# Kernel tuning notes

Measured on AMD Instinct MI355X. Metric: run time of the kernel, lower is better.

The kernel has to match this reference:

```python
import jax, jax.numpy as jnp
import numpy as np
from jax import lax

DIM = 128
HEADS = 8
B, H, W = 8, 128, 128


def conv1x1(w, x):
    # w: [out_c, in_c], x: [b, in_c, h, w]
    return jnp.einsum('oc,bchw->bohw', w, x)


def setup_inputs() -> dict:
    key = jax.random.key(0)
    ks = jax.random.split(key, 12)
    s = 0.02
    return {
        'x': jax.random.normal(ks[0], (B, DIM, H, W), dtype=jnp.float32),
        'W_qkv': jax.random.normal(ks[1], (3 * DIM, DIM), dtype=jnp.float32) * s,
        'W_dw': jax.random.normal(ks[2], (DIM, 1, 3, 3), dtype=jnp.float32) * s,
        'W_proj_s': jax.random.normal(ks[3], (DIM, DIM), dtype=jnp.float32) * s,
        'scale_s': jnp.ones((HEADS, 1, 1), dtype=jnp.float32),
        'W_ff1': jax.random.normal(ks[4], (DIM, DIM), dtype=jnp.float32) * s,
        'W_ff2': jax.random.normal(ks[5], (DIM, DIM), dtype=jnp.float32) * s,
        'W_proj_f': jax.random.normal(ks[6], (DIM, DIM), dtype=jnp.float32) * s,
        'W_gsf': jax.random.normal(ks[7], (DIM, DIM), dtype=jnp.float32) * s,
        'b_gsf': jnp.zeros((DIM,), dtype=jnp.float32),
        'W_gfs': jax.random.normal(ks[8], (DIM, DIM), dtype=jnp.float32) * s,
        'b_gfs': jnp.zeros((DIM,), dtype=jnp.float32),
    }


def reference(x, W_qkv, W_dw, W_proj_s, scale_s, W_ff1, W_ff2, W_proj_f,
              W_gsf, b_gsf, W_gfs, b_gfs):
    b, c, h, w = x.shape
    head = HEADS
    ch = c // head

    # --- channel self-attention branch ---
    qkv = conv1x1(W_qkv, x)                      # [b, 3c, h, w]
    q_s, k_s, v_s = jnp.split(qkv, 3, axis=1)
    v_s_conv = lax.conv_general_dilated(
        v_s, W_dw, window_strides=(1, 1), padding='SAME',
        feature_group_count=c,
        dimension_numbers=('NCHW', 'OIHW', 'NCHW'))  # depthwise 3x3

    q = q_s.reshape(b, head, ch, h * w)
    k = k_s.reshape(b, head, ch, h * w)
    v = v_s.reshape(b, head, ch, h * w)
    attn = jax.nn.softmax(jnp.einsum('bhcn,bhdn->bhcd', q, k) * scale_s, axis=-1)
    out_s = jnp.einsum('bhcd,bhdn->bhcn', attn, v).reshape(b, c, h, w)
    out_s = conv1x1(W_proj_s, out_s + v_s_conv)

    # --- frequency filter branch ---
    xf = jnp.fft.rfft2(x, norm='ortho')          # complex [b,c,h,w//2+1]
    spatial_weights = conv1x1(W_ff2, jax.nn.gelu(conv1x1(W_ff1, x), approximate=False))
    freq_weights = jnp.fft.rfft2(spatial_weights, norm='ortho')
    out_f = jnp.fft.irfft2(xf * freq_weights, s=(h, w), norm='ortho')
    out_f = conv1x1(W_proj_f, out_f)

    # --- sigmoid-gated fusion ---
    gate_f = jax.nn.sigmoid(conv1x1(W_gsf, out_s) + b_gsf[:, None, None])
    gate_s = jax.nn.sigmoid(conv1x1(W_gfs, out_f) + b_gfs[:, None, None])
    return x + out_s * gate_s + out_f * gate_f
```

## Files before the change

kernel.cpp:

```cpp
#include <hip/hip_runtime.h>
#include <hip/hip_bf16.h>
#include <math.h>

#define HW 16384

typedef __attribute__((ext_vector_type(8))) short bf16x8;
typedef __attribute__((ext_vector_type(4))) float f32x4;

__device__ __forceinline__ unsigned short f2bf(float a)
{
    __hip_bfloat16 h = __float2bfloat16(a);
    return __builtin_bit_cast(unsigned short, h);
}
__device__ __forceinline__ unsigned f2bf_pk(float a, float b)
{
    return (unsigned)f2bf(a) | ((unsigned)f2bf(b) << 16);
}
__device__ __forceinline__ float bf2f(unsigned short u)
{
    return __uint_as_float(((unsigned)u) << 16);
}
__device__ __forceinline__ float sigmoidf_(float v) { return 1.f / (1.f + expf(-v)); }

__device__ __forceinline__ float2 cmul(float2 a, float2 b)
{
    return make_float2(a.x * b.x - a.y * b.y, a.x * b.y + a.y * b.x);
}

__global__ __launch_bounds__(256)
void wprep_k(const float* __restrict__ w0, const float* __restrict__ w1,
             const float* __restrict__ w2, const float* __restrict__ w3,
             const float* __restrict__ w4, const float* __restrict__ w5,
             const float* __restrict__ w6, int4* __restrict__ Wbf4)
{
    int m = blockIdx.x >> 3;
    int slot = (blockIdx.x & 7) * 256 + threadIdx.x;
    const float* src;
    switch (m) {
        case 0: src = w0; break;
        case 1: src = w1; break;
        case 2: src = w2; break;
        case 3: src = w3; break;
        case 4: src = w4; break;
        case 5: src = w5; break;
        default: src = w6; break;
    }
    int o = slot >> 4;
    int c16 = (slot & 15) ^ (o & 7);
    const float* p = src + o * 128 + c16 * 8;
    int4 pk;
    pk.x = f2bf_pk(p[0], p[1]); pk.y = f2bf_pk(p[2], p[3]);
    pk.z = f2bf_pk(p[4], p[5]); pk.w = f2bf_pk(p[6], p[7]);
    Wbf4[m * 2048 + slot] = pk;
}

__global__ __launch_bounds__(256)
void conv_mfma_k(const float* __restrict__ in, const int4* __restrict__ wbf,
                 unsigned short* __restrict__ out)
{
    __shared__ short WL[128 * 128];
    __shared__ short XL[64 * 128];
    int t = threadIdx.x;
    int gb = blockIdx.x;
    int b = gb >> 8;
    int n0 = (gb & 255) << 6;

    #pragma unroll
    for (int it = 0; it < 8; ++it)
        ((int4*)WL)[it * 256 + t] = wbf[it * 256 + t];

    const float* inb = in + (size_t)b * 128 * HW + n0;
    int nl = t & 63;
    #pragma unroll
    for (int it = 0; it < 4; ++it) {
        int c8 = (t >> 6) + it * 4;
        float v[8];
        #pragma unroll
        for (int j = 0; j < 8; ++j) v[j] = inb[(size_t)(c8 * 8 + j) * HW + nl];
        int4 p;
        p.x = f2bf_pk(v[0], v[1]); p.y = f2bf_pk(v[2], v[3]);
        p.z = f2bf_pk(v[4], v[5]); p.w = f2bf_pk(v[6], v[7]);
        ((int4*)XL)[nl * 16 + (c8 ^ (nl & 7))] = p;
    }
    __syncthreads();

    int l = t & 63, w = t >> 6, kg = l >> 4, l15 = l & 15, l7 = l15 & 7;
    f32x4 acc[2][4];
    #pragma unroll
    for (int mf = 0; mf < 2; ++mf)
        #pragma unroll
        for (int nf = 0; nf < 4; ++nf) acc[mf][nf] = (f32x4){0.f, 0.f, 0.f, 0.f};
    #pragma unroll
    for (int ks = 0; ks < 4; ++ks) {
        int ch = ks * 4 + kg;
        bf16x8 A0 = ((const bf16x8*)WL)[(w * 32 + l15) * 16 + (ch ^ l7)];
        bf16x8 A1 = ((const bf16x8*)WL)[(w * 32 + 16 + l15) * 16 + (ch ^ l7)];
        #pragma unroll
        for (int nf = 0; nf < 4; ++nf) {
            bf16x8 Bf = ((const bf16x8*)XL)[(nf * 16 + l15) * 16 + (ch ^ l7)];
            acc[0][nf] = __builtin_amdgcn_mfma_f32_16x16x32_bf16(A0, Bf, acc[0][nf], 0, 0, 0);
            acc[1][nf] = __builtin_amdgcn_mfma_f32_16x16x32_bf16(A1, Bf, acc[1][nf], 0, 0, 0);
        }
    }
    #pragma unroll
    for (int mf = 0; mf < 2; ++mf)
        #pragma unroll
        for (int nf = 0; nf < 4; ++nf)
            #pragma unroll
            for (int i = 0; i < 4; ++i) {
                int row = w * 32 + mf * 16 + kg * 4 + i;
                int col = n0 + nf * 16 + l15;
                out[((size_t)b * 128 + row) * HW + col] = f2bf(acc[mf][nf][i]);
            }
}

__global__ __launch_bounds__(256)
void conv_mfma_bf_k(const unsigned short* __restrict__ in,
                    const int4* __restrict__ wbf,
                    unsigned short* __restrict__ out)
{
    __shared__ short WL[128 * 128];
    __shared__ short XL[64 * 128];
    int t = threadIdx.x;
    int gb = blockIdx.x;
    int b = gb >> 8;
    int n0 = (gb & 255) << 6;

    #pragma unroll
    for (int it = 0; it < 8; ++it)
        ((int4*)WL)[it * 256 + t] = wbf[it * 256 + t];

    const unsigned short* inb = in + (size_t)b * 128 * HW + n0;
    int nl = t & 63;
    #pragma unroll
    for (int it = 0; it < 4; ++it) {
        int c8 = (t >> 6) + it * 4;
        unsigned u[8];
        #pragma unroll
        for (int j = 0; j < 8; ++j) u[j] = inb[(size_t)(c8 * 8 + j) * HW + nl];
        int4 p;
        p.x = (int)(u[0] | (u[1] << 16)); p.y = (int)(u[2] | (u[3] << 16));
        p.z = (int)(u[4] | (u[5] << 16)); p.w = (int)(u[6] | (u[7] << 16));
        ((int4*)XL)[nl * 16 + (c8 ^ (nl & 7))] = p;
    }
    __syncthreads();

    int l = t & 63, w = t >> 6, kg = l >> 4, l15 = l & 15, l7 = l15 & 7;
    f32x4 acc[2][4];
    #pragma unroll
    for (int mf = 0; mf < 2; ++mf)
        #pragma unroll
        for (int nf = 0; nf < 4; ++nf) acc[mf][nf] = (f32x4){0.f, 0.f, 0.f, 0.f};
    #pragma unroll
    for (int ks = 0; ks < 4; ++ks) {
        int ch = ks * 4 + kg;
        bf16x8 A0 = ((const bf16x8*)WL)[(w * 32 + l15) * 16 + (ch ^ l7)];
        bf16x8 A1 = ((const bf16x8*)WL)[(w * 32 + 16 + l15) * 16 + (ch ^ l7)];
        #pragma unroll
        for (int nf = 0; nf < 4; ++nf) {
            bf16x8 Bf = ((const bf16x8*)XL)[(nf * 16 + l15) * 16 + (ch ^ l7)];
            acc[0][nf] = __builtin_amdgcn_mfma_f32_16x16x32_bf16(A0, Bf, acc[0][nf], 0, 0, 0);
            acc[1][nf] = __builtin_amdgcn_mfma_f32_16x16x32_bf16(A1, Bf, acc[1][nf], 0, 0, 0);
        }
    }
    #pragma unroll
    for (int mf = 0; mf < 2; ++mf)
        #pragma unroll
        for (int nf = 0; nf < 4; ++nf)
            #pragma unroll
            for (int i = 0; i < 4; ++i) {
                int row = w * 32 + mf * 16 + kg * 4 + i;
                int col = n0 + nf * 16 + l15;
                out[((size_t)b * 128 + row) * HW + col] = f2bf(acc[mf][nf][i]);
            }
}

__global__ __launch_bounds__(256)
void dwconv_k(const unsigned short* __restrict__ V, const float* __restrict__ Wdw,
              unsigned short* __restrict__ vcb)
{
    int tid = blockIdx.x * 256 + threadIdx.x;
    int e4 = tid & 4095;
    int bc = tid >> 12;
    int c = bc & 127;
    int y = e4 >> 5;
    int x0 = (e4 & 31) << 2;
    const unsigned short* vin = V + (size_t)bc * HW;
    float wf[9];
    #pragma unroll
    for (int i = 0; i < 9; ++i) wf[i] = Wdw[c * 9 + i];
    float a0 = 0.f, a1 = 0.f, a2 = 0.f, a3 = 0.f;
    #pragma unroll
    for (int dy = 0; dy < 3; ++dy) {
        int yy = y + dy - 1;
        if (yy < 0 || yy > 127) continue;
        const unsigned short* r = vin + yy * 128;
        uint2 mu = *(const uint2*)(r + x0);
        float m0 = bf2f((unsigned short)(mu.x & 0xFFFF));
        float m1 = bf2f((unsigned short)(mu.x >> 16));
        float m2 = bf2f((unsigned short)(mu.y & 0xFFFF));
        float m3 = bf2f((unsigned short)(mu.y >> 16));
        float left  = (x0 > 0)   ? bf2f(r[x0 - 1]) : 0.f;
        float right = (x0 < 124) ? bf2f(r[x0 + 4]) : 0.f;
        float w0 = wf[dy * 3], w1 = wf[dy * 3 + 1], w2 = wf[dy * 3 + 2];
        a0 += w0 * left + w1 * m0 + w2 * m1;
        a1 += w0 * m0   + w1 * m1 + w2 * m2;
        a2 += w0 * m1   + w1 * m2 + w2 * m3;
        a3 += w0 * m2   + w1 * m3 + w2 * right;
    }
    uint2 r2;
    r2.x = f2bf_pk(a0, a1);
    r2.y = f2bf_pk(a2, a3);
    *(uint2*)(vcb + (size_t)bc * HW + y * 128 + x0) = r2;
}

__global__ __launch_bounds__(256)
void gram_mfma_k(const float* __restrict__ x, float* __restrict__ Gp)
{
    __shared__ short XL[128 * 128];
    int t = threadIdx.x;
    int blk = blockIdx.x;
    int b = blk >> 5, ks = blk & 31;
    const float* xb = x + (size_t)b * 128 * HW + ks * 512;
    int l = t & 63, w = t >> 6, kg = l >> 4, l15 = l & 15, l7 = l15 & 7;

    f32x4 acc[2][8];
    #pragma unroll
    for (int mf = 0; mf < 2; ++mf)
        #pragma unroll
        for (int nf = 0; nf < 8; ++nf) acc[mf][nf] = (f32x4){0.f, 0.f, 0.f, 0.f};

    for (int kc = 0; kc < 4; ++kc) {
        __syncthreads();
        #pragma unroll
        for (int it = 0; it < 8; ++it) {
            int g = it * 256 + t;
            int row = g >> 4, oct = g & 15;
            const float* p = xb + (size_t)row * HW + kc * 128 + oct * 8;
            int4 pk;
            pk.x = f2bf_pk(p[0], p[1]); pk.y = f2bf_pk(p[2], p[3]);
            pk.z = f2bf_pk(p[4], p[5]); pk.w = f2bf_pk(p[6], p[7]);
            ((int4*)XL)[row * 16 + (oct ^ (row & 7))] = pk;
        }
        __syncthreads();
        #pragma unroll
        for (int s = 0; s < 4; ++s) {
            int oct = s * 4 + kg;
            bf16x8 A0 = ((const bf16x8*)XL)[(w * 32 + l15) * 16 + (oct ^ l7)];
            bf16x8 A1 = ((const bf16x8*)XL)[(w * 32 + 16 + l15) * 16 + (oct ^ l7)];
            #pragma unroll
            for (int nf = 0; nf < 8; ++nf) {
                bf16x8 Bf = ((const bf16x8*)XL)[(nf * 16 + l15) * 16 + (oct ^ l7)];
                acc[0][nf] = __builtin_amdgcn_mfma_f32_16x16x32_bf16(A0, Bf, acc[0][nf], 0, 0, 0);
                acc[1][nf] = __builtin_amdgcn_mfma_f32_16x16x32_bf16(A1, Bf, acc[1][nf], 0, 0, 0);
            }
        }
    }
    float* gp = Gp + (size_t)blk * 16384;
    #pragma unroll
    for (int mf = 0; mf < 2; ++mf)
        #pragma unroll
        for (int nf = 0; nf < 8; ++nf)
            #pragma unroll
            for (int i = 0; i < 4; ++i) {
                int row = w * 32 + mf * 16 + kg * 4 + i;
                int col = nf * 16 + l15;
                gp[row * 128 + col] = acc[mf][nf][i];
            }
}

__global__ void gram_reduce_k(const float* __restrict__ Gp, float* __restrict__ G)
{
    int idx = blockIdx.x * 256 + threadIdx.x;
    int b = idx >> 14;
    int ij = idx & 16383;
    const float* gp = Gp + (size_t)(b * 32) * 16384 + ij;
    float s = 0.f;
    #pragma unroll
    for (int ks = 0; ks < 32; ++ks) s += gp[(size_t)ks * 16384];
    G[idx] = s;
}

__global__ __launch_bounds__(256)
void attn_s2_k(const float* __restrict__ G, const float* __restrict__ Wqkv,
               const float* __restrict__ scale, float* __restrict__ S)
{
    __shared__ float Wq[16][129];
    __shared__ float Wk[16][129];
    __shared__ float Ts[16][129];
    int bh = blockIdx.x;
    int b = bh >> 3, h = bh & 7;
    int t = threadIdx.x;
    #pragma unroll
    for (int i = 0; i < 8; ++i) {
        int idx = t + i * 256;
        int r = idx >> 7, ci = idx & 127;
        Wq[r][ci] = Wqkv[(size_t)(h * 16 + r) * 128 + ci];
        Wk[r][ci] = Wqkv[(size_t)(128 + h * 16 + r) * 128 + ci];
    }
    __syncthreads();
    const float* Gb = G + (size_t)b * 16384;
    #pragma unroll
    for (int i = 0; i < 8; ++i) {
        int idx = t + i * 256;
        int c = idx >> 7, col = idx & 127;
        float s = 0.f;
        #pragma unroll 8
        for (int ci = 0; ci < 128; ++ci)
            s += Wq[c][ci] * Gb[ci * 128 + col];
        Ts[c][col] = s;
    }
    __syncthreads();
    int c = t >> 4, d = t & 15;
    float s = 0.f;
    #pragma unroll 8
    for (int col = 0; col < 128; ++col)
        s += Ts[c][col] * Wk[d][col];
    s *= scale[h];
    float m = s;
    #pragma unroll
    for (int w = 1; w < 16; w <<= 1)
        m = fmaxf(m, __shfl_xor(m, w, 64));
    float e = expf(s - m);
    float sum = e;
    #pragma unroll
    for (int w = 1; w < 16; w <<= 1)
        sum += __shfl_xor(sum, w, 64);
    S[(size_t)bh * 256 + t] = e / sum;
}

__global__ __launch_bounds__(256)
void proj_s_pv_k(const unsigned short* __restrict__ V,
                 const unsigned short* __restrict__ vcb,
                 const float* __restrict__ S, const int4* __restrict__ wbf,
                 unsigned short* __restrict__ out_s)
{
    __shared__ short WL[128 * 128];
    __shared__ short XL[64 * 128];
    __shared__ float SL[2048];
    int t = threadIdx.x;
    int gb = blockIdx.x;
    int b = gb >> 8;
    int n0 = (gb & 255) << 6;

    #pragma unroll
    for (int it = 0; it < 8; ++it)
        ((int4*)WL)[it * 256 + t] = wbf[it * 256 + t];
    #pragma unroll
    for (int i = 0; i < 8; ++i)
        SL[i * 256 + t] = S[(size_t)b * 2048 + i * 256 + t];
    __syncthreads();

    int col = t & 63, w = t >> 6;
    #pragma unroll
    for (int hh = 0; hh < 2; ++hh) {
        int h = w * 2 + hh;
        float v[16];
        #pragma unroll
        for (int d = 0; d < 16; ++d)
            v[d] = bf2f(V[((size_t)(b * 128 + h * 16 + d)) * HW + n0 + col]);
        float o[16];
        #pragma unroll
        for (int c = 0; c < 16; ++c) {
            const float* sl = SL + h * 256 + c * 16;
            float s = 0.f;
            #pragma unroll
            for (int d = 0; d < 16; ++d) s += sl[d] * v[d];
            o[c] = s + bf2f(vcb[((size_t)(b * 128 + h * 16 + c)) * HW + n0 + col]);
        }
        #pragma unroll
        for (int oc = 0; oc < 2; ++oc) {
            int octet = h * 2 + oc;
            int4 p;
            p.x = f2bf_pk(o[oc * 8 + 0], o[oc * 8 + 1]);
            p.y = f2bf_pk(o[oc * 8 + 2], o[oc * 8 + 3]);
            p.z = f2bf_pk(o[oc * 8 + 4], o[oc * 8 + 5]);
            p.w = f2bf_pk(o[oc * 8 + 6], o[oc * 8 + 7]);
            ((int4*)XL)[col * 16 + (octet ^ (col & 7))] = p;
        }
    }
    __syncthreads();

    int l = t & 63, kg = l >> 4, l15 = l & 15, l7 = l15 & 7;
    f32x4 acc[2][4];
    #pragma unroll
    for (int mf = 0; mf < 2; ++mf)
        #pragma unroll
        for (int nf = 0; nf < 4; ++nf) acc[mf][nf] = (f32x4){0.f, 0.f, 0.f, 0.f};
    #pragma unroll
    for (int ks = 0; ks < 4; ++ks) {
        int ch = ks * 4 + kg;
        bf16x8 A0 = ((const bf16x8*)WL)[(w * 32 + l15) * 16 + (ch ^ l7)];
        bf16x8 A1 = ((const bf16x8*)WL)[(w * 32 + 16 + l15) * 16 + (ch ^ l7)];
        #pragma unroll
        for (int nf = 0; nf < 4; ++nf) {
            bf16x8 Bf = ((const bf16x8*)XL)[(nf * 16 + l15) * 16 + (ch ^ l7)];
            acc[0][nf] = __builtin_amdgcn_mfma_f32_16x16x32_bf16(A0, Bf, acc[0][nf], 0, 0, 0);
            acc[1][nf] = __builtin_amdgcn_mfma_f32_16x16x32_bf16(A1, Bf, acc[1][nf], 0, 0, 0);
        }
    }
    #pragma unroll
    for (int mf = 0; mf < 2; ++mf)
        #pragma unroll
        for (int nf = 0; nf < 4; ++nf)
            #pragma unroll
            for (int i = 0; i < 4; ++i) {
                int row = w * 32 + mf * 16 + kg * 4 + i;
                int colg = n0 + nf * 16 + l15;
                out_s[((size_t)b * 128 + row) * HW + colg] = f2bf(acc[mf][nf][i]);
            }
}

__global__ __launch_bounds__(256)
void ff_fused_k(const float* __restrict__ x, const int4* __restrict__ w1bf,
                const int4* __restrict__ w2bf, unsigned short* __restrict__ outp)
{
    __shared__ short WL[128 * 128];
    __shared__ short XL[64 * 128];
    int t = threadIdx.x;
    int gb = blockIdx.x;
    int b = gb >> 8;
    int n0 = (gb & 255) << 6;

    #pragma unroll
    for (int it = 0; it < 8; ++it)
        ((int4*)WL)[it * 256 + t] = w1bf[it * 256 + t];

    const float* inb = x + (size_t)b * 128 * HW + n0;
    int nl = t & 63;
    #pragma unroll
    for (int it = 0; it < 4; ++it) {
        int c8 = (t >> 6) + it * 4;
        float v[8];
        #pragma unroll
        for (int j = 0; j < 8; ++j) v[j] = inb[(size_t)(c8 * 8 + j) * HW + nl];
        int4 p;
        p.x = f2bf_pk(v[0], v[1]); p.y = f2bf_pk(v[2], v[3]);
        p.z = f2bf_pk(v[4], v[5]); p.w = f2bf_pk(v[6], v[7]);
        ((int4*)XL)[nl * 16 + (c8 ^ (nl & 7))] = p;
    }
    __syncthreads();

    int l = t & 63, w = t >> 6, kg = l >> 4, l15 = l & 15, l7 = l15 & 7;
    f32x4 acc[2][4];
    #pragma unroll
    for (int mf = 0; mf < 2; ++mf)
        #pragma unroll
        for (int nf = 0; nf < 4; ++nf) acc[mf][nf] = (f32x4){0.f, 0.f, 0.f, 0.f};
    #pragma unroll
    for (int ks = 0; ks < 4; ++ks) {
        int ch = ks * 4 + kg;
        bf16x8 A0 = ((const bf16x8*)WL)[(w * 32 + l15) * 16 + (ch ^ l7)];
        bf16x8 A1 = ((const bf16x8*)WL)[(w * 32 + 16 + l15) * 16 + (ch ^ l7)];
        #pragma unroll
        for (int nf = 0; nf < 4; ++nf) {
            bf16x8 Bf = ((const bf16x8*)XL)[(nf * 16 + l15) * 16 + (ch ^ l7)];
            acc[0][nf] = __builtin_amdgcn_mfma_f32_16x16x32_bf16(A0, Bf, acc[0][nf], 0, 0, 0);
            acc[1][nf] = __builtin_amdgcn_mfma_f32_16x16x32_bf16(A1, Bf, acc[1][nf], 0, 0, 0);
        }
    }
    __syncthreads();

    #pragma unroll
    for (int it = 0; it < 8; ++it)
        ((int4*)WL)[it * 256 + t] = w2bf[it * 256 + t];
    #pragma unroll
    for (int mf = 0; mf < 2; ++mf)
        #pragma unroll
        for (int nf = 0; nf < 4; ++nf) {
            float g4[4];
            #pragma unroll
            for (int i = 0; i < 4; ++i) {
                float v = acc[mf][nf][i];
                g4[i] = 0.5f * v * (1.0f + erff(v * 0.70710678118654752f));
            }
            int col = nf * 16 + l15;
            int r0 = w * 32 + mf * 16 + kg * 4;
            int octet = r0 >> 3;
            uint2 pk2;
            pk2.x = f2bf_pk(g4[0], g4[1]);
            pk2.y = f2bf_pk(g4[2], g4[3]);
            ((uint2*)XL)[(col * 16 + (octet ^ (col & 7))) * 2 + (kg & 1)] = pk2;
        }
    __syncthreads();

    f32x4 acc2[2][4];
    #pragma unroll
    for (int mf = 0; mf < 2; ++mf)
        #pragma unroll
        for (int nf = 0; nf < 4; ++nf) acc2[mf][nf] = (f32x4){0.f, 0.f, 0.f, 0.f};
    #pragma unroll
    for (int ks = 0; ks < 4; ++ks) {
        int ch = ks * 4 + kg;
        bf16x8 A0 = ((const bf16x8*)WL)[(w * 32 + l15) * 16 + (ch ^ l7)];
        bf16x8 A1 = ((const bf16x8*)WL)[(w * 32 + 16 + l15) * 16 + (ch ^ l7)];
        #pragma unroll
        for (int nf = 0; nf < 4; ++nf) {
            bf16x8 Bf = ((const bf16x8*)XL)[(nf * 16 + l15) * 16 + (ch ^ l7)];
            acc2[0][nf] = __builtin_amdgcn_mfma_f32_16x16x32_bf16(A0, Bf, acc2[0][nf], 0, 0, 0);
            acc2[1][nf] = __builtin_amdgcn_mfma_f32_16x16x32_bf16(A1, Bf, acc2[1][nf], 0, 0, 0);
        }
    }
    #pragma unroll
    for (int mf = 0; mf < 2; ++mf)
        #pragma unroll
        for (int nf = 0; nf < 4; ++nf)
            #pragma unroll
            for (int i = 0; i < 4; ++i) {
                int row = w * 32 + mf * 16 + kg * 4 + i;
                int col = n0 + nf * 16 + l15;
                outp[((size_t)b * 128 + row) * HW + col] = f2bf(acc2[mf][nf][i]);
            }
}

__global__ __launch_bounds__(256)
void fuse2_k(const float* __restrict__ x, const unsigned short* __restrict__ outs,
             const unsigned short* __restrict__ outf,
             const int4* __restrict__ wgsf_bf, const float* __restrict__ bgsf,
             const int4* __restrict__ wgfs_bf, const float* __restrict__ bgfs,
             float* __restrict__ out)
{
    __shared__ short WS[64 * 128];
    __shared__ short WF[64 * 128];
    __shared__ short XS[64 * 128];
    __shared__ short XF[64 * 128];
    int t = threadIdx.x;
    int gb = blockIdx.x;
    int half = gb & 1;
    int nt = (gb >> 1) & 255;
    int b = gb >> 9;
    int n0 = nt << 6;

    #pragma unroll
    for (int it = 0; it < 4; ++it) {
        ((int4*)WS)[it * 256 + t] = wgsf_bf[half * 1024 + it * 256 + t];
        ((int4*)WF)[it * 256 + t] = wgfs_bf[half * 1024 + it * 256 + t];
    }
    const unsigned short* sb = outs + (size_t)b * 128 * HW + n0;
    const unsigned short* fb = outf + (size_t)b * 128 * HW + n0;
    int nl = t & 63;
    #pragma unroll
    for (int it = 0; it < 4; ++it) {
        int c8 = (t >> 6) + it * 4;
        unsigned us[8], uf[8];
        #pragma unroll
        for (int j = 0; j < 8; ++j) {
            size_t a = (size_t)(c8 * 8 + j) * HW + nl;
            us[j] = sb[a];
            uf[j] = fb[a];
        }
        int4 ps, pf;
        ps.x = (int)(us[0] | (us[1] << 16)); ps.y = (int)(us[2] | (us[3] << 16));
        ps.z = (int)(us[4] | (us[5] << 16)); ps.w = (int)(us[6] | (us[7] << 16));
        pf.x = (int)(uf[0] | (uf[1] << 16)); pf.y = (int)(uf[2] | (uf[3] << 16));
        pf.z = (int)(uf[4] | (uf[5] << 16)); pf.w = (int)(uf[6] | (uf[7] << 16));
        ((int4*)XS)[nl * 16 + (c8 ^ (nl & 7))] = ps;
        ((int4*)XF)[nl * 16 + (c8 ^ (nl & 7))] = pf;
    }
    __syncthreads();

    int l = t & 63, w = t >> 6, kg = l >> 4, l15 = l & 15, l7 = l15 & 7;
    f32x4 aS[4], aF[4];
    #pragma unroll
    for (int nf = 0; nf < 4; ++nf) {
        aS[nf] = (f32x4){0.f, 0.f, 0.f, 0.f};
        aF[nf] = (f32x4){0.f, 0.f, 0.f, 0.f};
    }
    #pragma unroll
    for (int ks = 0; ks < 4; ++ks) {
        int ch = ks * 4 + kg;
        bf16x8 As = ((const bf16x8*)WS)[(w * 16 + l15) * 16 + (ch ^ l7)];
        bf16x8 Af = ((const bf16x8*)WF)[(w * 16 + l15) * 16 + (ch ^ l7)];
        #pragma unroll
        for (int nf = 0; nf < 4; ++nf) {
            bf16x8 Bs = ((const bf16x8*)XS)[(nf * 16 + l15) * 16 + (ch ^ l7)];
            bf16x8 Bf = ((const bf16x8*)XF)[(nf * 16 + l15) * 16 + (ch ^ l7)];
            aS[nf] = __builtin_amdgcn_mfma_f32_16x16x32_bf16(As, Bs, aS[nf], 0, 0, 0);
            aF[nf] = __builtin_amdgcn_mfma_f32_16x16x32_bf16(Af, Bf, aF[nf], 0, 0, 0);
        }
    }
    #pragma unroll
    for (int nf = 0; nf < 4; ++nf)
        #pragma unroll
        for (int i = 0; i < 4; ++i) {
            int row = half * 64 + w * 16 + kg * 4 + i;
            int cc = nf * 16 + l15;
            float gf = sigmoidf_(aS[nf][i] + bgsf[row]);
            float gs = sigmoidf_(aF[nf][i] + bgfs[row]);
            size_t gi = ((size_t)(b * 128) + row) * HW + n0 + cc;
            float os = bf2f(outs[gi]);
            float of = bf2f(outf[gi]);
            out[gi] = x[gi] + os * gs + of * gf;
        }
}

__device__ __forceinline__ int ZIX(int r, int j)
{
    return r * 128 + (j ^ ((r & 3) << 3) ^ (((j >> 4) & 3) << 1));
}
__device__ __forceinline__ float2 zld(const unsigned* Z, int r, int j)
{
    unsigned z = Z[ZIX(r, j)];
    return make_float2(bf2f((unsigned short)(z & 0xFFFF)),
                       bf2f((unsigned short)(z >> 16)));
}
__device__ __forceinline__ void zst(unsigned* Z, int r, int j, float2 v)
{
    Z[ZIX(r, j)] = f2bf_pk(v.x, v.y);
}

__device__ __forceinline__ void dft16(float2* v)
{
    const float C1 = 0.92387953251f, S1 = 0.38268343236f, R2 = 0.70710678119f;
    const float2 W16[8] = {
        {1.f, 0.f}, {C1, -S1}, {R2, -R2}, {S1, -C1},
        {0.f, -1.f}, {-S1, -C1}, {-R2, -R2}, {-C1, -S1}};
    #pragma unroll
    for (int i = 0; i < 8; ++i) {
        float2 a = v[i], b = v[i + 8];
        v[i] = make_float2(a.x + b.x, a.y + b.y);
        float2 d = make_float2(a.x - b.x, a.y - b.y);
        v[i + 8] = cmul(d, W16[i]);
    }
    #pragma unroll
    for (int blk = 0; blk < 16; blk += 8)
        #pragma unroll
        for (int i = 0; i < 4; ++i) {
            float2 a = v[blk + i], b = v[blk + i + 4];
            v[blk + i] = make_float2(a.x + b.x, a.y + b.y);
            float2 d = make_float2(a.x - b.x, a.y - b.y);
            v[blk + i + 4] = cmul(d, W16[2 * i]);
        }
    #pragma unroll
    for (int blk = 0; blk < 16; blk += 4) {
        float2 a0 = v[blk], b0 = v[blk + 2];
        v[blk] = make_float2(a0.x + b0.x, a0.y + b0.y);
        v[blk + 2] = make_float2(a0.x - b0.x, a0.y - b0.y);
        float2 a1 = v[blk + 1], b1 = v[blk + 3];
        v[blk + 1] = make_float2(a1.x + b1.x, a1.y + b1.y);
        float2 d = make_float2(a1.x - b1.x, a1.y - b1.y);
        v[blk + 3] = make_float2(d.y, -d.x);
    }
    #pragma unroll
    for (int blk = 0; blk < 16; blk += 2) {
        float2 a = v[blk], b = v[blk + 1];
        v[blk] = make_float2(a.x + b.x, a.y + b.y);
        v[blk + 1] = make_float2(a.x - b.x, a.y - b.y);
    }
}

__device__ __forceinline__ void dft8(float2* v)
{
    const float R2 = 0.70710678119f;
    const float2 W8[4] = {{1.f, 0.f}, {R2, -R2}, {0.f, -1.f}, {-R2, -R2}};
    #pragma unroll
    for (int i = 0; i < 4; ++i) {
        float2 a = v[i], b = v[i + 4];
        v[i] = make_float2(a.x + b.x, a.y + b.y);
        float2 d = make_float2(a.x - b.x, a.y - b.y);
        v[i + 4] = cmul(d, W8[i]);
    }
    #pragma unroll
    for (int blk = 0; blk < 8; blk += 4) {
        float2 a0 = v[blk], b0 = v[blk + 2];
        v[blk] = make_float2(a0.x + b0.x, a0.y + b0.y);
        v[blk + 2] = make_float2(a0.x - b0.x, a0.y - b0.y);
        float2 a1 = v[blk + 1], b1 = v[blk + 3];
        v[blk + 1] = make_float2(a1.x + b1.x, a1.y + b1.y);
        float2 d = make_float2(a1.x - b1.x, a1.y - b1.y);
        v[blk + 3] = make_float2(d.y, -d.x);
    }
    #pragma unroll
    for (int blk = 0; blk < 8; blk += 2) {
        float2 a = v[blk], b = v[blk + 1];
        v[blk] = make_float2(a.x + b.x, a.y + b.y);
        v[blk + 1] = make_float2(a.x - b.x, a.y - b.y);
    }
}

__device__ __forceinline__ void fft_line_row(unsigned* Z, const float2* tw,
                                             int row, int n2)
{
    const int BREV4[16] = {0,8,4,12,2,10,6,14,1,9,5,13,3,11,7,15};
    const int BREV3[8] = {0,4,2,6,1,5,3,7};
    float2 v[16];
    #pragma unroll
    for (int n1 = 0; n1 < 16; ++n1) v[n1] = zld(Z, row, 8 * n1 + n2);
    dft16(v);
    #pragma unroll
    for (int p = 0; p < 16; ++p) {
        int k1 = BREV4[p];
        zst(Z, row, 16 * n2 + k1, cmul(v[p], tw[n2 * k1]));
    }
    float2 wa[8], wb[8];
    #pragma unroll
    for (int m = 0; m < 8; ++m) {
        wa[m] = zld(Z, row, 16 * m + n2);
        wb[m] = zld(Z, row, 16 * m + n2 + 8);
    }
    dft8(wa);
    dft8(wb);
    #pragma unroll
    for (int p = 0; p < 8; ++p) {
        zst(Z, row, n2 + 16 * BREV3[p], wa[p]);
        zst(Z, row, n2 + 8 + 16 * BREV3[p], wb[p]);
    }
}

__device__ __forceinline__ void fft_line_col(unsigned* Z, const float2* tw,
                                             int col, int n2)
{
    const int BREV4[16] = {0,8,4,12,2,10,6,14,1,9,5,13,3,11,7,15};
    const int BREV3[8] = {0,4,2,6,1,5,3,7};
    float2 v[16];
    #pragma unroll
    for (int n1 = 0; n1 < 16; ++n1) v[n1] = zld(Z, 8 * n1 + n2, col);
    dft16(v);
    #pragma unroll
    for (int p = 0; p < 16; ++p) {
        int k1 = BREV4[p];
        zst(Z, 16 * n2 + k1, col, cmul(v[p], tw[n2 * k1]));
    }
    float2 wa[8], wb[8];
    #pragma unroll
    for (int m = 0; m < 8; ++m) {
        wa[m] = zld(Z, 16 * m + n2, col);
        wb[m] = zld(Z, 16 * m + n2 + 8, col);
    }
    dft8(wa);
    dft8(wb);
    #pragma unroll
    for (int p = 0; p < 8; ++p) {
        zst(Z, n2 + 16 * BREV3[p], col, wa[p]);
        zst(Z, n2 + 8 + 16 * BREV3[p], col, wb[p]);
    }
}

__global__ __launch_bounds__(256)
void fft_all_k(const float* __restrict__ x, const unsigned short* __restrict__ sw,
               unsigned short* __restrict__ outp)
{
    __shared__ unsigned Z[128 * 128];
    __shared__ float2 tw[128];
    const int BREV3[8] = {0,4,2,6,1,5,3,7};
    int t = threadIdx.x;
    if (t < 128) {
        float sn, cs;
        sincosf(0.049087385212340519f * (float)t, &sn, &cs);
        tw[t] = make_float2(cs, -sn);
    }
    size_t base = (size_t)blockIdx.x * HW;

    for (int i = 0; i < 64; ++i) {
        int idx = t + i * 256;
        int r = idx >> 7, j = idx & 127;
        Z[ZIX(r, j)] = (unsigned)f2bf(x[base + idx]) |
                       ((unsigned)sw[base + idx] << 16);
    }
    __syncthreads();

    int ln = t >> 3, n2 = t & 7;
    #pragma unroll
    for (int it = 0; it < 4; ++it) fft_line_row(Z, tw, it * 32 + ln, n2);
    __syncthreads();
    #pragma unroll
    for (int it = 0; it < 4; ++it) fft_line_col(Z, tw, it * 32 + ln, n2);
    __syncthreads();

    for (int item = t; item < 8194; item += 256) {
        int rA, kA, rB, kB;
        if (item < 8064) {
            rA = 1 + (item >> 7); kA = item & 127;
            rB = 128 - rA; kB = (128 - kA) & 127;
        } else {
            int it2 = item - 8064;
            rA = rB = (it2 < 65) ? 0 : 64;
            kA = (it2 < 65) ? it2 : (it2 - 65);
            kB = (128 - kA) & 127;
        }
        float2 z1 = zld(Z, rA, kA);
        float2 z2 = zld(Z, rB, kB);
        float2 X = make_float2(0.5f * (z1.x + z2.x), 0.5f * (z1.y - z2.y));
        float Dx = z1.x - z2.x, Dy = z1.y + z2.y;
        float2 Wf = make_float2(0.5f * Dy, -0.5f * Dx);
        float2 Y = cmul(X, Wf);
        zst(Z, rA, kA, make_float2(Y.x, -Y.y));
        zst(Z, rB, kB, Y);
    }
    __syncthreads();

    #pragma unroll
    for (int it = 0; it < 4; ++it) fft_line_col(Z, tw, it * 32 + ln, n2);
    __syncthreads();

    const float scale = 1.f / 2097152.f;
    const int BREV4[16] = {0,8,4,12,2,10,6,14,1,9,5,13,3,11,7,15};
    #pragma unroll
    for (int it = 0; it < 4; ++it) {
        int row = it * 32 + ln;
        float2 v[16];
        #pragma unroll
        for (int n1 = 0; n1 < 16; ++n1) v[n1] = zld(Z, row, 8 * n1 + n2);
        dft16(v);
        #pragma unroll
        for (int p = 0; p < 16; ++p) {
            int k1 = BREV4[p];
            zst(Z, row, 16 * n2 + k1, cmul(v[p], tw[n2 * k1]));
        }
        float2 wa[8], wb[8];
        #pragma unroll
        for (int m = 0; m < 8; ++m) {
            wa[m] = zld(Z, row, 16 * m + n2);
            wb[m] = zld(Z, row, 16 * m + n2 + 8);
        }
        dft8(wa);
        dft8(wb);
        #pragma unroll
        for (int p = 0; p < 8; ++p) {
            outp[base + row * 128 + n2 + 16 * BREV3[p]] = f2bf(wa[p].x * scale);
            outp[base + row * 128 + n2 + 8 + 16 * BREV3[p]] = f2bf(wb[p].x * scale);
        }
    }
}

extern "C" void kernel_launch(void* const* d_in, const int* in_sizes, int n_in,
                              void* d_out, int out_size, void* d_ws, size_t ws_size,
                              hipStream_t stream)
{
    const float* x        = (const float*)d_in[0];
    const float* W_qkv    = (const float*)d_in[1];
    const float* W_dw     = (const float*)d_in[2];
    const float* W_proj_s = (const float*)d_in[3];
    const float* scale_s  = (const float*)d_in[4];
    const float* W_ff1    = (const float*)d_in[5];
    const float* W_ff2    = (const float*)d_in[6];
    const float* W_proj_f = (const float*)d_in[7];
    const float* W_gsf    = (const float*)d_in[8];
    const float* b_gsf    = (const float*)d_in[9];
    const float* W_gfs    = (const float*)d_in[10];
    const float* b_gfs    = (const float*)d_in[11];
    float* out = (float*)d_out;

    char* ws = (char*)d_ws;
    const size_t MB32 = 33554432ull;
    const size_t MB64 = 67108864ull;
    const size_t MB96 = 100663296ull;
    unsigned short* V     = (unsigned short*)(ws);
    unsigned short* out_s = (unsigned short*)(ws + MB32);
    unsigned short* swb   = (unsigned short*)(ws + MB64);
    unsigned short* pre   = (unsigned short*)(ws + MB64);
    unsigned short* out_fp= (unsigned short*)(ws);
    int4* Wbf4            = (int4*)(ws + MB96);
    unsigned short* vcb   = (unsigned short*)out;
    float* Gp  = out + 8388608;
    float* G   = out + 8388608 + 4194304;
    float* S   = G + 131072;

    wprep_k<<<56, 256, 0, stream>>>(W_qkv + 256 * 128, W_proj_s, W_ff1, W_ff2,
                                    W_proj_f, W_gsf, W_gfs, Wbf4);

    conv_mfma_k<<<2048, 256, 0, stream>>>(x, Wbf4 + 0 * 2048, V);
    dwconv_k<<<16384, 256, 0, stream>>>(V, W_dw, vcb);
    gram_mfma_k<<<256, 256, 0, stream>>>(x, Gp);
    gram_reduce_k<<<512, 256, 0, stream>>>(Gp, G);
    attn_s2_k<<<64, 256, 0, stream>>>(G, W_qkv, scale_s, S);
    proj_s_pv_k<<<2048, 256, 0, stream>>>(V, vcb, S, Wbf4 + 1 * 2048, out_s);

    ff_fused_k<<<2048, 256, 0, stream>>>(x, Wbf4 + 2 * 2048, Wbf4 + 3 * 2048, swb);
    fft_all_k<<<1024, 256, 0, stream>>>(x, swb, pre);
    conv_mfma_bf_k<<<2048, 256, 0, stream>>>(pre, Wbf4 + 4 * 2048, out_fp);

    fuse2_k<<<4096, 256, 0, stream>>>(x, out_s, out_fp,
                                      Wbf4 + 5 * 2048, b_gsf,
                                      Wbf4 + 6 * 2048, b_gfs, out);
}
```

Before: 332.3 us.

## Fuse V projection and FF MLP into one head kernel, remap fuse2 blocks by XCD

Merges the V 1x1-conv kernel and the two-layer GELU feed-forward kernel into a single head kernel. The kernel converts each x tile to bf16 in LDS once and reuses it for both GEMM chains, so x is read from global memory once instead of twice and one launch is removed. It also remaps fuse2 block indices so that consecutive tiles land on the same XCD, and fully unrolls the FFT load loop. In exchange, the fused kernel uses more LDS per block (separate input and intermediate buffers), which may reduce occupancy.

```diff
diff --git a/kernel.cpp b/kernel.cpp
--- a/kernel.cpp
+++ b/kernel.cpp
@@ -55,11 +55,13 @@
 }
 
 __global__ __launch_bounds__(256)
-void conv_mfma_k(const float* __restrict__ in, const int4* __restrict__ wbf,
-                 unsigned short* __restrict__ out)
+void head_k(const float* __restrict__ x, const int4* __restrict__ wv,
+            const int4* __restrict__ w1, const int4* __restrict__ w2,
+            unsigned short* __restrict__ V, unsigned short* __restrict__ swb)
 {
     __shared__ short WL[128 * 128];
-    __shared__ short XL[64 * 128];
+    __shared__ short XLx[64 * 128];
+    __shared__ short XM[64 * 128];
     int t = threadIdx.x;
     int gb = blockIdx.x;
     int b = gb >> 8;
@@ -67,9 +69,9 @@
 
     #pragma unroll
     for (int it = 0; it < 8; ++it)
-        ((int4*)WL)[it * 256 + t] = wbf[it * 256 + t];
-
-    const float* inb = in + (size_t)b * 128 * HW + n0;
+        ((int4*)WL)[it * 256 + t] = wv[it * 256 + t];
+
+    const float* inb = x + (size_t)b * 128 * HW + n0;
     int nl = t & 63;
     #pragma unroll
     for (int it = 0; it < 4; ++it) {
@@ -80,11 +82,12 @@
         int4 p;
         p.x = f2bf_pk(v[0], v[1]); p.y = f2bf_pk(v[2], v[3]);
         p.z = f2bf_pk(v[4], v[5]); p.w = f2bf_pk(v[6], v[7]);
-        ((int4*)XL)[nl * 16 + (c8 ^ (nl & 7))] = p;
+        ((int4*)XLx)[nl * 16 + (c8 ^ (nl & 7))] = p;
     }
     __syncthreads();
 
     int l = t & 63, w = t >> 6, kg = l >> 4, l15 = l & 15, l7 = l15 & 7;
+
     f32x4 acc[2][4];
     #pragma unroll
     for (int mf = 0; mf < 2; ++mf)
@@ -97,7 +100,7 @@
         bf16x8 A1 = ((const bf16x8*)WL)[(w * 32 + 16 + l15) * 16 + (ch ^ l7)];
         #pragma unroll
         for (int nf = 0; nf < 4; ++nf) {
-            bf16x8 Bf = ((const bf16x8*)XL)[(nf * 16 + l15) * 16 + (ch ^ l7)];
+            bf16x8 Bf = ((const bf16x8*)XLx)[(nf * 16 + l15) * 16 + (ch ^ l7)];
             acc[0][nf] = __builtin_amdgcn_mfma_f32_16x16x32_bf16(A0, Bf, acc[0][nf], 0, 0, 0);
             acc[1][nf] = __builtin_amdgcn_mfma_f32_16x16x32_bf16(A1, Bf, acc[1][nf], 0, 0, 0);
         }
@@ -110,7 +113,82 @@
             for (int i = 0; i < 4; ++i) {
                 int row = w * 32 + mf * 16 + kg * 4 + i;
                 int col = n0 + nf * 16 + l15;
-                out[((size_t)b * 128 + row) * HW + col] = f2bf(acc[mf][nf][i]);
+                V[((size_t)b * 128 + row) * HW + col] = f2bf(acc[mf][nf][i]);
+            }
+    __syncthreads();
+
+    #pragma unroll
+    for (int it = 0; it < 8; ++it)
+        ((int4*)WL)[it * 256 + t] = w1[it * 256 + t];
+    __syncthreads();
+
+    #pragma unroll
+    for (int mf = 0; mf < 2; ++mf)
+        #pragma unroll
+        for (int nf = 0; nf < 4; ++nf) acc[mf][nf] = (f32x4){0.f, 0.f, 0.f, 0.f};
+    #pragma unroll
+    for (int ks = 0; ks < 4; ++ks) {
+        int ch = ks * 4 + kg;
+        bf16x8 A0 = ((const bf16x8*)WL)[(w * 32 + l15) * 16 + (ch ^ l7)];
+        bf16x8 A1 = ((const bf16x8*)WL)[(w * 32 + 16 + l15) * 16 + (ch ^ l7)];
+        #pragma unroll
+        for (int nf = 0; nf < 4; ++nf) {
+            bf16x8 Bf = ((const bf16x8*)XLx)[(nf * 16 + l15) * 16 + (ch ^ l7)];
+            acc[0][nf] = __builtin_amdgcn_mfma_f32_16x16x32_bf16(A0, Bf, acc[0][nf], 0, 0, 0);
+            acc[1][nf] = __builtin_amdgcn_mfma_f32_16x16x32_bf16(A1, Bf, acc[1][nf], 0, 0, 0);
+        }
+    }
+    __syncthreads();
+
+    #pragma unroll
+    for (int it = 0; it < 8; ++it)
+        ((int4*)WL)[it * 256 + t] = w2[it * 256 + t];
+    #pragma unroll
+    for (int mf = 0; mf < 2; ++mf)
+        #pragma unroll
+        for (int nf = 0; nf < 4; ++nf) {
+            float g4[4];
+            #pragma unroll
+            for (int i = 0; i < 4; ++i) {
+                float v = acc[mf][nf][i];
+                g4[i] = 0.5f * v * (1.0f + erff(v * 0.70710678118654752f));
+            }
+            int col = nf * 16 + l15;
+            int r0 = w * 32 + mf * 16 + kg * 4;
+            int octet = r0 >> 3;
+            uint2 pk2;
+            pk2.x = f2bf_pk(g4[0], g4[1]);
+            pk2.y = f2bf_pk(g4[2], g4[3]);
+            ((uint2*)XM)[(col * 16 + (octet ^ (col & 7))) * 2 + (kg & 1)] = pk2;
+        }
+    __syncthreads();
+
+    f32x4 acc2[2][4];
+    #pragma unroll
+    for (int mf = 0; mf < 2; ++mf)
+        #pragma unroll
+        for (int nf = 0; nf < 4; ++nf) acc2[mf][nf] = (f32x4){0.f, 0.f, 0.f, 0.f};
+    #pragma unroll
+    for (int ks = 0; ks < 4; ++ks) {
+        int ch = ks * 4 + kg;
+        bf16x8 A0 = ((const bf16x8*)WL)[(w * 32 + l15) * 16 + (ch ^ l7)];
+        bf16x8 A1 = ((const bf16x8*)WL)[(w * 32 + 16 + l15) * 16 + (ch ^ l7)];
+        #pragma unroll
+        for (int nf = 0; nf < 4; ++nf) {
+            bf16x8 Bf = ((const bf16x8*)XM)[(nf * 16 + l15) * 16 + (ch ^ l7)];
+            acc2[0][nf] = __builtin_amdgcn_mfma_f32_16x16x32_bf16(A0, Bf, acc2[0][nf], 0, 0, 0);
+            acc2[1][nf] = __builtin_amdgcn_mfma_f32_16x16x32_bf16(A1, Bf, acc2[1][nf], 0, 0, 0);
+        }
+    }
+    #pragma unroll
+    for (int mf = 0; mf < 2; ++mf)
+        #pragma unroll
+        for (int nf = 0; nf < 4; ++nf)
+            #pragma unroll
+            for (int i = 0; i < 4; ++i) {
+                int row = w * 32 + mf * 16 + kg * 4 + i;
+                int col = n0 + nf * 16 + l15;
+                swb[((size_t)b * 128 + row) * HW + col] = f2bf(acc2[mf][nf][i]);
             }
 }
 
@@ -412,108 +490,6 @@
 }
 
 __global__ __launch_bounds__(256)
-void ff_fused_k(const float* __restrict__ x, const int4* __restrict__ w1bf,
-                const int4* __restrict__ w2bf, unsigned short* __restrict__ outp)
-{
-    __shared__ short WL[128 * 128];
-    __shared__ short XL[64 * 128];
-    int t = threadIdx.x;
-    int gb = blockIdx.x;
-    int b = gb >> 8;
-    int n0 = (gb & 255) << 6;
-
-    #pragma unroll
-    for (int it = 0; it < 8; ++it)
-        ((int4*)WL)[it * 256 + t] = w1bf[it * 256 + t];
-
-    const float* inb = x + (size_t)b * 128 * HW + n0;
-    int nl = t & 63;
-    #pragma unroll
-    for (int it = 0; it < 4; ++it) {
-        int c8 = (t >> 6) + it * 4;
-        float v[8];
-        #pragma unroll
-        for (int j = 0; j < 8; ++j) v[j] = inb[(size_t)(c8 * 8 + j) * HW + nl];
-        int4 p;
-        p.x = f2bf_pk(v[0], v[1]); p.y = f2bf_pk(v[2], v[3]);
-        p.z = f2bf_pk(v[4], v[5]); p.w = f2bf_pk(v[6], v[7]);
-        ((int4*)XL)[nl * 16 + (c8 ^ (nl & 7))] = p;
-    }
-    __syncthreads();
-
-    int l = t & 63, w = t >> 6, kg = l >> 4, l15 = l & 15, l7 = l15 & 7;
-    f32x4 acc[2][4];
-    #pragma unroll
-    for (int mf = 0; mf < 2; ++mf)
-        #pragma unroll
-        for (int nf = 0; nf < 4; ++nf) acc[mf][nf] = (f32x4){0.f, 0.f, 0.f, 0.f};
-    #pragma unroll
-    for (int ks = 0; ks < 4; ++ks) {
-        int ch = ks * 4 + kg;
-        bf16x8 A0 = ((const bf16x8*)WL)[(w * 32 + l15) * 16 + (ch ^ l7)];
-        bf16x8 A1 = ((const bf16x8*)WL)[(w * 32 + 16 + l15) * 16 + (ch ^ l7)];
-        #pragma unroll
-        for (int nf = 0; nf < 4; ++nf) {
-            bf16x8 Bf = ((const bf16x8*)XL)[(nf * 16 + l15) * 16 + (ch ^ l7)];
-            acc[0][nf] = __builtin_amdgcn_mfma_f32_16x16x32_bf16(A0, Bf, acc[0][nf], 0, 0, 0);
-            acc[1][nf] = __builtin_amdgcn_mfma_f32_16x16x32_bf16(A1, Bf, acc[1][nf], 0, 0, 0);
-        }
-    }
-    __syncthreads();
-
-    #pragma unroll
-    for (int it = 0; it < 8; ++it)
-        ((int4*)WL)[it * 256 + t] = w2bf[it * 256 + t];
-    #pragma unroll
-    for (int mf = 0; mf < 2; ++mf)
-        #pragma unroll
-        for (int nf = 0; nf < 4; ++nf) {
-            float g4[4];
-            #pragma unroll
-            for (int i = 0; i < 4; ++i) {
-                float v = acc[mf][nf][i];
-                g4[i] = 0.5f * v * (1.0f + erff(v * 0.70710678118654752f));
-            }
-            int col = nf * 16 + l15;
-            int r0 = w * 32 + mf * 16 + kg * 4;
-            int octet = r0 >> 3;
-            uint2 pk2;
-            pk2.x = f2bf_pk(g4[0], g4[1]);
-            pk2.y = f2bf_pk(g4[2], g4[3]);
-            ((uint2*)XL)[(col * 16 + (octet ^ (col & 7))) * 2 + (kg & 1)] = pk2;
-        }
-    __syncthreads();
-
-    f32x4 acc2[2][4];
-    #pragma unroll
-    for (int mf = 0; mf < 2; ++mf)
-        #pragma unroll
-        for (int nf = 0; nf < 4; ++nf) acc2[mf][nf] = (f32x4){0.f, 0.f, 0.f, 0.f};
-    #pragma unroll
-    for (int ks = 0; ks < 4; ++ks) {
-        int ch = ks * 4 + kg;
-        bf16x8 A0 = ((const bf16x8*)WL)[(w * 32 + l15) * 16 + (ch ^ l7)];
-        bf16x8 A1 = ((const bf16x8*)WL)[(w * 32 + 16 + l15) * 16 + (ch ^ l7)];
-        #pragma unroll
-        for (int nf = 0; nf < 4; ++nf) {
-            bf16x8 Bf = ((const bf16x8*)XL)[(nf * 16 + l15) * 16 + (ch ^ l7)];
-            acc2[0][nf] = __builtin_amdgcn_mfma_f32_16x16x32_bf16(A0, Bf, acc2[0][nf], 0, 0, 0);
-            acc2[1][nf] = __builtin_amdgcn_mfma_f32_16x16x32_bf16(A1, Bf, acc2[1][nf], 0, 0, 0);
-        }
-    }
-    #pragma unroll
-    for (int mf = 0; mf < 2; ++mf)
-        #pragma unroll
-        for (int nf = 0; nf < 4; ++nf)
-            #pragma unroll
-            for (int i = 0; i < 4; ++i) {
-                int row = w * 32 + mf * 16 + kg * 4 + i;
-                int col = n0 + nf * 16 + l15;
-                outp[((size_t)b * 128 + row) * HW + col] = f2bf(acc2[mf][nf][i]);
-            }
-}
-
-__global__ __launch_bounds__(256)
 void fuse2_k(const float* __restrict__ x, const unsigned short* __restrict__ outs,
              const unsigned short* __restrict__ outf,
              const int4* __restrict__ wgsf_bf, const float* __restrict__ bgsf,
@@ -526,10 +502,11 @@
     __shared__ short XF[64 * 128];
     int t = threadIdx.x;
     int gb = blockIdx.x;
-    int half = gb & 1;
-    int nt = (gb >> 1) & 255;
-    int b = gb >> 9;
-    int n0 = nt << 6;
+    int xcd = gb & 7, ii = gb >> 3;
+    int T = xcd * 256 + (ii >> 1);
+    int half = ii & 1;
+    int b = T >> 8;
+    int n0 = (T & 255) << 6;
 
     #pragma unroll
     for (int it = 0; it < 4; ++it) {
@@ -751,6 +728,7 @@
     }
     size_t base = (size_t)blockIdx.x * HW;
 
+    #pragma unroll
     for (int i = 0; i < 64; ++i) {
         int idx = t + i * 256;
         int r = idx >> 7, j = idx & 127;
@@ -859,14 +837,15 @@
     wprep_k<<<56, 256, 0, stream>>>(W_qkv + 256 * 128, W_proj_s, W_ff1, W_ff2,
                                     W_proj_f, W_gsf, W_gfs, Wbf4);
 
-    conv_mfma_k<<<2048, 256, 0, stream>>>(x, Wbf4 + 0 * 2048, V);
+    head_k<<<2048, 256, 0, stream>>>(x, Wbf4 + 0 * 2048, Wbf4 + 2 * 2048,
+                                     Wbf4 + 3 * 2048, V, swb);
+
     dwconv_k<<<16384, 256, 0, stream>>>(V, W_dw, vcb);
     gram_mfma_k<<<256, 256, 0, stream>>>(x, Gp);
     gram_reduce_k<<<512, 256, 0, stream>>>(Gp, G);
     attn_s2_k<<<64, 256, 0, stream>>>(G, W_qkv, scale_s, S);
     proj_s_pv_k<<<2048, 256, 0, stream>>>(V, vcb, S, Wbf4 + 1 * 2048, out_s);
 
-    ff_fused_k<<<2048, 256, 0, stream>>>(x, Wbf4 + 2 * 2048, Wbf4 + 3 * 2048, swb);
     fft_all_k<<<1024, 256, 0, stream>>>(x, swb, pre);
     conv_mfma_bf_k<<<2048, 256, 0, stream>>>(pre, Wbf4 + 4 * 2048, out_fp);
 
```

Measured after the change: 317.4 us. -4.5%, faster.
